# Optimization experiments

Measured on AMD Instinct MI355X. Metric: run time of the kernel, lower is better.

## Reference

```python
import jax, jax.numpy as jnp
import numpy as np
import math

D_MODEL = 2048
H = 16
Q_LORA = 1536
KV_LORA = 512
DN = 128   # qk_nope_head_dim
DR = 64    # qk_rope_head_dim
DV = 128   # v_head_dim
B, S = 2, 2048
EPS = 1e-5


def layernorm(x, g, b):
    mu = jnp.mean(x, axis=-1, keepdims=True)
    var = jnp.mean(jnp.square(x - mu), axis=-1, keepdims=True)
    return (x - mu) * jax.lax.rsqrt(var + EPS) * g + b


def rope_cos_sin(position_ids, dim):
    inv_freq = 1.0 / (10000.0 ** (jnp.arange(0, dim, 2, dtype=jnp.float32) / dim))
    ang = position_ids.astype(jnp.float32)[:, None] * inv_freq[None, :]  # [S, dim/2]
    return jnp.cos(ang), jnp.sin(ang)


def apply_rope(x, cos, sin):
    # x: [..., S, ..., dim]; cos/sin broadcastable [..., S, ..., dim/2]
    x1, x2 = jnp.split(x, 2, axis=-1)
    return jnp.concatenate([x1 * cos - x2 * sin, x1 * sin + x2 * cos], axis=-1)


def setup_inputs() -> dict:
    key = jax.random.key(0)
    ks = jax.random.split(key, 8)
    sc = 0.02
    return {
        "hidden_states": jax.random.normal(ks[0], (B, S, D_MODEL), jnp.float32),
        "w_qa": jax.random.normal(ks[1], (Q_LORA, D_MODEL), jnp.float32) * sc,
        "ln_qa_g": jnp.ones((Q_LORA,), jnp.float32),
        "ln_qa_b": jnp.zeros((Q_LORA,), jnp.float32),
        "w_qb": jax.random.normal(ks[2], (H * DN, Q_LORA), jnp.float32) * sc,
        "w_qrope": jax.random.normal(ks[3], (H * DR, Q_LORA), jnp.float32) * sc,
        "w_kva": jax.random.normal(ks[4], (KV_LORA + DR, D_MODEL), jnp.float32) * sc,
        "ln_kva_g": jnp.ones((KV_LORA,), jnp.float32),
        "ln_kva_b": jnp.zeros((KV_LORA,), jnp.float32),
        "w_kvb": jax.random.normal(ks[5], (H * (DN + DV), KV_LORA), jnp.float32) * sc,
        "w_o": jax.random.normal(ks[6], (D_MODEL, H * DV), jnp.float32) * sc,
        "position_ids": jnp.arange(S, dtype=jnp.int32),
    }


def reference(hidden_states, w_qa, ln_qa_g, ln_qa_b, w_qb, w_qrope,
              w_kva, ln_kva_g, ln_kva_b, w_kvb, w_o, position_ids):
    bsz, seq_len, _ = hidden_states.shape

    # --- Q path (low-rank) ---
    q_latent = layernorm(hidden_states @ w_qa.T, ln_qa_g, ln_qa_b)        # [B,S,Q_LORA]
    q_nope = (q_latent @ w_qb.T).reshape(bsz, seq_len, H, DN)             # [B,S,H,DN]
    q_rope = (q_latent @ w_qrope.T).reshape(bsz, seq_len, H, DR)          # [B,S,H,DR]

    # --- absorb k up-projection into q ---
    k_up = w_kvb[: H * DN].reshape(H, DN, KV_LORA)
    v_up = w_kvb[H * DN:].reshape(H, DV, KV_LORA)
    q_abs = jnp.einsum('bshd,hdr->bshr', q_nope, k_up)                    # [B,S,H,R]

    # --- KV latent path ---
    kv_mixed = hidden_states @ w_kva.T                                    # [B,S,R+DR]
    kv_latent = layernorm(kv_mixed[..., :KV_LORA], ln_kva_g, ln_kva_b)    # [B,S,R]
    k_rope = kv_mixed[..., KV_LORA:]                                      # [B,S,DR]

    # --- RoPE ---
    cos, sin = rope_cos_sin(position_ids, DR)                             # [S,DR/2]
    q_rope = apply_rope(q_rope, cos[None, :, None, :], sin[None, :, None, :])
    k_rope = apply_rope(k_rope, cos[None, :, :], sin[None, :, :])

    # --- attention over latent channel (keys shared across heads) ---
    q_full = jnp.concatenate([q_abs, q_rope], axis=-1)                    # [B,S,H,R+DR]
    k_full = jnp.concatenate([kv_latent, k_rope], axis=-1)                # [B,S,R+DR]
    scale = 1.0 / math.sqrt(DN + DR)
    scores = jnp.einsum('bqhc,bkc->bhqk', q_full, k_full) * scale
    probs = jax.nn.softmax(scores, axis=-1)
    attn = jnp.einsum('bhqk,bkr->bhqr', probs, kv_latent)                 # [B,H,S,R]

    # --- absorbed v up-projection + output ---
    attn_v = jnp.einsum('bhqr,hvr->bqhv', attn, v_up)                     # [B,S,H,DV]
    attn_v = attn_v.reshape(bsz, seq_len, H * DV)
    return attn_v @ w_o.T                                                 # [B,S,D_MODEL]
```

## Files before the change

kernel.cpp:

```cpp
#include <hip/hip_runtime.h>
#include <math.h>

#define D_MODEL 2048
#define NH 16
#define Q_LORA 1536
#define KV_LORA 512
#define DN 128
#define DR 64
#define DV 128
#define BB 2
#define SS 2048
#define NROWS (BB*SS)
#define LN_EPS 1e-5f

typedef __attribute__((ext_vector_type(8))) short short8;
typedef __attribute__((ext_vector_type(4))) float f32x4;

__device__ __forceinline__ ushort f2bf(float f) {
    unsigned int u = __float_as_uint(f);
    u = u + 0x7fffu + ((u >> 16) & 1u);
    return (ushort)(u >> 16);
}

__device__ __forceinline__ float fexp2(float x) {
#if __has_builtin(__builtin_amdgcn_exp2f)
    return __builtin_amdgcn_exp2f(x);
#else
    return exp2f(x);
#endif
}

__device__ __forceinline__ void cv4(const float* __restrict__ s,
                                    ushort* __restrict__ d, long i) {
    float4 v = ((const float4*)s)[i];
    ushort4 o;
    o.x = f2bf(v.x); o.y = f2bf(v.y); o.z = f2bf(v.z); o.w = f2bf(v.w);
    ((ushort4*)d)[i] = o;
}

__global__ __launch_bounds__(256)
void cvt_all(const float* __restrict__ hs,     const float* __restrict__ w_qa,
             const float* __restrict__ w_qb,   const float* __restrict__ w_qrope,
             const float* __restrict__ w_kvb,  const float* __restrict__ w_kva,
             ushort* __restrict__ hs_bf,       ushort* __restrict__ w_qa_bf,
             ushort* __restrict__ w_qb_bf,     ushort* __restrict__ w_qrope_bf,
             ushort* __restrict__ w_kvb_bf,    ushort* __restrict__ w_kva_bf,
             const int* __restrict__ pos,      float2* __restrict__ tab)
{
    long i = (long)blockIdx.x * 256 + threadIdx.x;
    if (i < 2097152) { cv4(hs, hs_bf, i); return; }
    i -= 2097152;
    if (i < 786432) { cv4(w_qa, w_qa_bf, i); return; }
    i -= 786432;
    if (i < 786432) { cv4(w_qb, w_qb_bf, i); return; }
    i -= 786432;
    if (i < 393216) { cv4(w_qrope, w_qrope_bf, i); return; }
    i -= 393216;
    if (i < 524288) { cv4(w_kvb, w_kvb_bf, i); return; }
    i -= 524288;
    if (i < 327680) {
        long e = i * 4;
        int row = (int)(e >> 11), col = (int)(e & 2047);
        ushort4 o;
        if (row < 576) {
            float4 v = *(const float4*)(w_kva + (long)row * 2048 + col);
            o.x = f2bf(v.x); o.y = f2bf(v.y); o.z = f2bf(v.z); o.w = f2bf(v.w);
        } else { o.x = 0; o.y = 0; o.z = 0; o.w = 0; }
        *(ushort4*)(w_kva_bf + (long)row * 2048 + col) = o;
        return;
    }
    i -= 327680;
    if (i >= 65536) return;
    int idx = (int)i;
    int fi = idx & 31;
    int s = idx >> 5;
    double ang = (double)pos[s] * exp(-(double)fi * 0.28782313662425572);
    float2 cs;
    cs.x = (float)cos(ang);
    cs.y = (float)sin(ang);
    tab[idx] = cs;
}

#define GLL16(g, l) \
    __builtin_amdgcn_global_load_lds((const __attribute__((address_space(1))) void*)(g), \
                                     (__attribute__((address_space(3))) void*)(l), 16, 0, 0)

__device__ __forceinline__ void gemm_core(const ushort* __restrict__ A,
    const ushort* __restrict__ Bp, ushort* As, ushort* Bs,
    int K, int lda, int ldb, int m0, int n0, int tid, f32x4 acc[4][4])
{
    int l = tid & 63, w = tid >> 6;
    int l15 = l & 15, quad = l >> 4;
    int wm = (w >> 1) * 64, wn = (w & 1) * 64;
    int ob = tid * 16;
    int row = ob >> 6, colb = ob & 63;
    const char* ga0 = (const char*)(A  + (long)(m0 + row) * lda)      + colb;
    const char* ga1 = (const char*)(A  + (long)(m0 + row + 64) * lda) + colb;
    const char* gb0 = (const char*)(Bp + (long)(n0 + row) * ldb)      + colb;
    const char* gb1 = (const char*)(Bp + (long)(n0 + row + 64) * ldb) + colb;
    ushort* la0 = As + tid * 8;
    ushort* la1 = As + 2048 + tid * 8;
    ushort* lb0 = Bs + tid * 8;
    ushort* lb1 = Bs + 2048 + tid * 8;

    for (int k0 = 0; k0 < K; k0 += 32) {
        GLL16(ga0, la0); GLL16(ga1, la1);
        GLL16(gb0, lb0); GLL16(gb1, lb1);
        ga0 += 64; ga1 += 64; gb0 += 64; gb1 += 64;
        __syncthreads();
        short8 af[4], bf[4];
        #pragma unroll
        for (int i = 0; i < 4; ++i)
            af[i] = *(const short8*)(As + (wm + i * 16 + l15) * 32 + quad * 8);
        #pragma unroll
        for (int j = 0; j < 4; ++j)
            bf[j] = *(const short8*)(Bs + (wn + j * 16 + l15) * 32 + quad * 8);
        #pragma unroll
        for (int i = 0; i < 4; ++i)
            #pragma unroll
            for (int j = 0; j < 4; ++j)
                acc[i][j] = __builtin_amdgcn_mfma_f32_16x16x32_bf16(
                    af[i], bf[j], acc[i][j], 0, 0, 0);
        __syncthreads();
    }
}

__global__ __launch_bounds__(256)
void gemm_f32out(const ushort* __restrict__ A, const ushort* __restrict__ B,
                 float* __restrict__ C, int K, int lda, int ldb, int ldc)
{
    __shared__ __align__(16) ushort As[128 * 32];
    __shared__ __align__(16) ushort Bs[128 * 32];
    int tid = threadIdx.x;
    int m0 = blockIdx.y * 128, n0 = blockIdx.x * 128;
    f32x4 acc[4][4] = {};
    gemm_core(A, B, As, Bs, K, lda, ldb, m0, n0, tid, acc);
    int l = tid & 63, w = tid >> 6;
    int l15 = l & 15, quad = l >> 4;
    int wm = (w >> 1) * 64, wn = (w & 1) * 64;
    #pragma unroll
    for (int i = 0; i < 4; ++i)
        #pragma unroll
        for (int j = 0; j < 4; ++j)
            #pragma unroll
            for (int r = 0; r < 4; ++r) {
                long gm = m0 + wm + i * 16 + quad * 4 + r;
                long gn = n0 + wn + j * 16 + l15;
                C[gm * ldc + gn] = acc[i][j][r];
            }
}

__global__ __launch_bounds__(256)
void gemm_dual(const ushort* __restrict__ A, const ushort* __restrict__ Bqa,
               const ushort* __restrict__ Bkva, float* __restrict__ Cq,
               float* __restrict__ Ckv)
{
    __shared__ __align__(16) ushort As[128 * 32];
    __shared__ __align__(16) ushort Bs[128 * 32];
    int tid = threadIdx.x;
    int bx = blockIdx.x;
    int m0 = blockIdx.y * 128;
    const ushort* Bp; float* C; int ldc, n0;
    if (bx < 12) { n0 = bx * 128;        Bp = Bqa  + (long)n0 * 2048; C = Cq;  ldc = 1536; }
    else         { n0 = (bx - 12) * 128; Bp = Bkva + (long)n0 * 2048; C = Ckv; ldc = 640; }
    f32x4 acc[4][4] = {};
    gemm_core(A, Bp, As, Bs, D_MODEL, D_MODEL, D_MODEL, m0, 0, tid, acc);
    int l = tid & 63, w = tid >> 6;
    int l15 = l & 15, quad = l >> 4;
    int wm = (w >> 1) * 64, wn = (w & 1) * 64;
    #pragma unroll
    for (int i = 0; i < 4; ++i)
        #pragma unroll
        for (int j = 0; j < 4; ++j)
            #pragma unroll
            for (int r = 0; r < 4; ++r) {
                long gm = m0 + wm + i * 16 + quad * 4 + r;
                long gn = n0 + wn + j * 16 + l15;
                C[gm * ldc + gn] = acc[i][j][r];
            }
}

__global__ __launch_bounds__(256)
void gemm_qkv(const ushort* __restrict__ Aq, const ushort* __restrict__ Bqb,
              const ushort* __restrict__ Bqr, ushort* __restrict__ qfull,
              const float2* __restrict__ tab,
              const ushort* __restrict__ Akv, const ushort* __restrict__ Bkvb,
              ushort* __restrict__ kfull, ushort* __restrict__ vt)
{
    __shared__ __align__(16) ushort As[128 * 32];
    __shared__ __align__(16) ushort Bs[128 * 32];
    int tid = threadIdx.x;
    int bx = blockIdx.x;
    int m0 = blockIdx.y * 128;
    int l = tid & 63, w = tid >> 6;
    int l15 = l & 15, quad = l >> 4;
    int wm = (w >> 1) * 64, wn = (w & 1) * 64;
    f32x4 acc[4][4] = {};

    if (bx < 24) {
        int n0 = bx * 128;
        const ushort* Bp = (n0 < 2048) ? Bqb + (long)n0 * Q_LORA
                                       : Bqr + (long)(n0 - 2048) * Q_LORA;
        gemm_core(Aq, Bp, As, Bs, Q_LORA, Q_LORA, Q_LORA, m0, 0, tid, acc);
        if (n0 < 2048) {
            int head = n0 >> 7;
            #pragma unroll
            for (int i = 0; i < 4; ++i)
                #pragma unroll
                for (int j = 0; j < 4; ++j)
                    #pragma unroll
                    for (int r = 0; r < 4; ++r) {
                        long gm = m0 + wm + i * 16 + quad * 4 + r;
                        int c = wn + j * 16 + l15;
                        qfull[(gm * NH + head) * 192 + c] = f2bf(acc[i][j][r]);
                    }
        } else {
            int nb = n0 - 2048;
            int head = (nb + wn) >> 6;
            #pragma unroll
            for (int i = 0; i < 4; ++i)
                #pragma unroll
                for (int j = 0; j < 2; ++j)
                    #pragma unroll
                    for (int r = 0; r < 4; ++r) {
                        long gm = m0 + wm + i * 16 + quad * 4 + r;
                        int ir = j * 16 + l15;
                        int s = (int)(gm & (SS - 1));
                        float2 cs = tab[s * 32 + ir];
                        float x1 = acc[i][j][r], x2 = acc[i][j + 2][r];
                        ushort* op = qfull + (gm * NH + head) * 192 + 128;
                        op[ir]      = f2bf(x1 * cs.x - x2 * cs.y);
                        op[ir + 32] = f2bf(x1 * cs.y + x2 * cs.x);
                    }
        }
    } else {
        int n0 = (bx - 24) * 128;
        const ushort* Bp = Bkvb + (long)n0 * KV_LORA;
        gemm_core(Akv, Bp, As, Bs, KV_LORA, KV_LORA, KV_LORA, m0, 0, tid, acc);
        if (n0 < 2048) {
            int head = n0 >> 7;
            #pragma unroll
            for (int i = 0; i < 4; ++i)
                #pragma unroll
                for (int j = 0; j < 4; ++j)
                    #pragma unroll
                    for (int r = 0; r < 4; ++r) {
                        long gm = m0 + wm + i * 16 + quad * 4 + r;
                        int c = wn + j * 16 + l15;
                        kfull[(gm * NH + head) * 192 + c] = f2bf(acc[i][j][r]);
                    }
        } else {
            int head = (n0 >> 7) - 16;
            #pragma unroll
            for (int i = 0; i < 4; ++i)
                #pragma unroll
                for (int j = 0; j < 4; ++j) {
                    long gm0 = m0 + wm + i * 16 + quad * 4;
                    int c = wn + j * 16 + l15;
                    ushort4 p;
                    p.x = f2bf(acc[i][j][0]); p.y = f2bf(acc[i][j][1]);
                    p.z = f2bf(acc[i][j][2]); p.w = f2bf(acc[i][j][3]);
                    *(ushort4*)(vt + (long)head * 128 * 4096 + (long)c * 4096 + gm0) = p;
                }
        }
    }
}

__global__ __launch_bounds__(256)
void ln_rope(const float* __restrict__ qlf, ushort* __restrict__ qlbf,
             const float* __restrict__ gqa, const float* __restrict__ bqa,
             const float* __restrict__ kvm, ushort* __restrict__ kvbf,
             const float* __restrict__ gkv, const float* __restrict__ bkv,
             ushort* __restrict__ kfull, const float2* __restrict__ tab,
             const float* __restrict__ w_o, ushort* __restrict__ w_o_bf)
{
    __shared__ float sred[4], ssred[4];
    int bid = blockIdx.x, tid = threadIdx.x;
    if (bid < 2 * NROWS) {
        const float* x; ushort* y; const float* g; const float* b; int n;
        if (bid < NROWS) {
            x = qlf + (long)bid * Q_LORA; y = qlbf + (long)bid * Q_LORA;
            g = gqa; b = bqa; n = Q_LORA;
        } else {
            int r = bid - NROWS;
            x = kvm + (long)r * 640; y = kvbf + (long)r * KV_LORA;
            g = gkv; b = bkv; n = KV_LORA;
        }
        float s = 0.f, ss = 0.f;
        for (int i = tid; i < n; i += 256) { float v = x[i]; s += v; ss += v * v; }
        #pragma unroll
        for (int off = 32; off > 0; off >>= 1) {
            s  += __shfl_xor(s, off);
            ss += __shfl_xor(ss, off);
        }
        int wid = tid >> 6, lane = tid & 63;
        if (lane == 0) { sred[wid] = s; ssred[wid] = ss; }
        __syncthreads();
        s  = sred[0] + sred[1] + sred[2] + sred[3];
        ss = ssred[0] + ssred[1] + ssred[2] + ssred[3];
        float mu  = s / n;
        float var = ss / n - mu * mu;
        float r = 1.0f / sqrtf(var + LN_EPS);
        for (int i = tid; i < n; i += 256)
            y[i] = f2bf((x[i] - mu) * r * g[i] + b[i]);
        return;
    }
    if (bid < 2 * NROWS + 512) {
        long idx = (long)(bid - 2 * NROWS) * 256 + tid;
        if (idx >= (long)NROWS * 32) return;
        int i = (int)(idx & 31);
        long rowi = idx >> 5;
        int s = (int)(rowi & (SS - 1));
        float2 cs = tab[s * 32 + i];
        float c = cs.x, sn = cs.y;
        const float* p = kvm + rowi * 640 + 512;
        float x1 = p[i], x2 = p[i + 32];
        ushort v1 = f2bf(x1 * c - x2 * sn);
        ushort v2 = f2bf(x1 * sn + x2 * c);
        ushort* o = kfull + rowi * NH * 192 + 128;
        #pragma unroll
        for (int h = 0; h < NH; ++h) {
            o[h * 192 + i]      = v1;
            o[h * 192 + i + 32] = v2;
        }
        return;
    }
    long i = (long)(bid - (2 * NROWS + 512)) * 256 + tid;
    if (i < 1048576) cv4(w_o, w_o_bf, i);
}

#define C2LOG 0.10412700456539414f
#define THR2  11.541560327111707f

__global__ __launch_bounds__(512, 4)
void flash_mfma(const ushort* __restrict__ qf, const ushort* __restrict__ kf,
                const ushort* __restrict__ vt, ushort* __restrict__ attnv)
{
    __shared__ __align__(16) ushort Ks[64 * 192];
    __shared__ __align__(16) ushort Vs[144 * 64];
    __shared__ __align__(16) ushort Ps[128 * 72];
    int tid = threadIdx.x;
    int w = tid >> 6, l = tid & 63, l15 = l & 15, quad = l >> 4;
    int bh = blockIdx.x;
    int b = bh >> 4, h = bh & 15;
    int q0 = blockIdx.y * 128;

    {
        int e = 8192 + tid * 2;
        ushort2 iv;
        iv.x = (e     < 8256) ? (ushort)0x3F80 : (ushort)0;
        iv.y = (e + 1 < 8256) ? (ushort)0x3F80 : (ushort)0;
        *(ushort2*)&Vs[e] = iv;
    }

    const ushort* qp = qf + ((long)(b * SS + q0 + 16 * w + l15) * NH + h) * 192 + quad * 8;
    short8 aq[6];
    #pragma unroll
    for (int kk = 0; kk < 6; ++kk) aq[kk] = *(const short8*)(qp + kk * 32);

    f32x4 o[8] = {};
    f32x4 osum = {};
    float mrow = -INFINITY;

    const ushort* kbase = kf + ((long)(b * SS) * NH + h) * 192;
    const ushort* vbase = vt + (long)h * 128 * 4096 + (long)b * SS;

    int r0k = tid >> 3, subk = tid & 7;
    int v0  = tid >> 2, subv = tid & 3;
    const ushort* kgp = kbase + (long)r0k * (NH * 192);
    const ushort* vgp = vbase + (long)v0 * 4096;

    short8 pk[3], pv[2];
    #pragma unroll
    for (int it = 0; it < 3; ++it)
        pk[it] = *(const short8*)(kgp + (subk + 8 * it) * 8);
    #pragma unroll
    for (int it = 0; it < 2; ++it)
        pv[it] = *(const short8*)(vgp + (subv + 4 * it) * 8);

    int ksw = r0k & 7, vsw = v0 & 7;

    for (int k0 = 0; k0 < SS; k0 += 64) {
        __syncthreads();
        #pragma unroll
        for (int it = 0; it < 3; ++it)
            *(short8*)&Ks[r0k * 192 + ((subk + 8 * it) ^ ksw) * 8] = pk[it];
        #pragma unroll
        for (int it = 0; it < 2; ++it)
            *(short8*)&Vs[v0 * 64 + ((subv + 4 * it) ^ vsw) * 8] = pv[it];
        __syncthreads();
        if (k0 + 64 < SS) {
            const ushort* kg = kgp + (long)(k0 + 64) * (NH * 192);
            const ushort* vg = vgp + (k0 + 64);
            #pragma unroll
            for (int it = 0; it < 3; ++it)
                pk[it] = *(const short8*)(kg + (subk + 8 * it) * 8);
            #pragma unroll
            for (int it = 0; it < 2; ++it)
                pv[it] = *(const short8*)(vg + (subv + 4 * it) * 8);
        }

        f32x4 sc[4] = {};
        __builtin_amdgcn_s_setprio(1);
        #pragma unroll
        for (int kk = 0; kk < 6; ++kk) {
            #pragma unroll
            for (int j = 0; j < 4; ++j) {
                int krow = j * 16 + l15;
                short8 kfr = *(const short8*)&Ks[krow * 192 + (((kk * 4 + quad) ^ (krow & 7))) * 8];
                sc[j] = __builtin_amdgcn_mfma_f32_16x16x32_bf16(kfr, aq[kk], sc[j], 0, 0, 0);
            }
        }
        __builtin_amdgcn_s_setprio(0);

        float rmax = fmaxf(
            fmaxf(fmaxf(fmaxf(sc[0][0], sc[0][1]), fmaxf(sc[0][2], sc[0][3])),
                  fmaxf(fmaxf(sc[1][0], sc[1][1]), fmaxf(sc[1][2], sc[1][3]))),
            fmaxf(fmaxf(fmaxf(sc[2][0], sc[2][1]), fmaxf(sc[2][2], sc[2][3])),
                  fmaxf(fmaxf(sc[3][0], sc[3][1]), fmaxf(sc[3][2], sc[3][3]))));
        rmax = fmaxf(rmax, __shfl_xor(rmax, 16));
        rmax = fmaxf(rmax, __shfl_xor(rmax, 32));
        float pmax = rmax * C2LOG;

        if (__any(pmax > mrow + THR2)) {
            float mnew = fmaxf(mrow, pmax);
            float alpha = fexp2(mrow - mnew);
            mrow = mnew;
            float a0 = __shfl(alpha, quad * 4 + 0);
            float a1 = __shfl(alpha, quad * 4 + 1);
            float a2 = __shfl(alpha, quad * 4 + 2);
            float a3 = __shfl(alpha, quad * 4 + 3);
            #pragma unroll
            for (int v8 = 0; v8 < 8; ++v8) {
                o[v8][0] *= a0; o[v8][1] *= a1;
                o[v8][2] *= a2; o[v8][3] *= a3;
            }
            osum[0] *= a0; osum[1] *= a1; osum[2] *= a2; osum[3] *= a3;
        }

        int prow = (16 * w + l15) * 72 + quad * 4;
        #pragma unroll
        for (int j = 0; j < 4; ++j) {
            float p0 = fexp2(fmaf(sc[j][0], C2LOG, -mrow));
            float p1 = fexp2(fmaf(sc[j][1], C2LOG, -mrow));
            float p2 = fexp2(fmaf(sc[j][2], C2LOG, -mrow));
            float p3 = fexp2(fmaf(sc[j][3], C2LOG, -mrow));
            uint2 pu;
            pu.x = (uint)f2bf(p0) | ((uint)f2bf(p1) << 16);
            pu.y = (uint)f2bf(p2) | ((uint)f2bf(p3) << 16);
            *(uint2*)&Ps[prow + j * 16] = pu;
        }

        __builtin_amdgcn_s_setprio(1);
        #pragma unroll
        for (int ks = 0; ks < 2; ++ks) {
            short8 pa = *(const short8*)&Ps[(16 * w + l15) * 72 + ks * 32 + quad * 8];
            #pragma unroll
            for (int v8 = 0; v8 < 8; ++v8) {
                int vrow = v8 * 16 + l15;
                short8 bv = *(const short8*)&Vs[vrow * 64 + (((ks * 4 + quad) ^ (vrow & 7))) * 8];
                o[v8] = __builtin_amdgcn_mfma_f32_16x16x32_bf16(pa, bv, o[v8], 0, 0, 0);
            }
            {
                int vrow = 128 + l15;
                short8 bv = *(const short8*)&Vs[vrow * 64 + (((ks * 4 + quad) ^ (vrow & 7))) * 8];
                osum = __builtin_amdgcn_mfma_f32_16x16x32_bf16(pa, bv, osum, 0, 0, 0);
            }
        }
        __builtin_amdgcn_s_setprio(0);
    }

    #pragma unroll
    for (int r = 0; r < 4; ++r) {
        float lsum = __shfl(osum[r], l & 48);
        float inv = 1.0f / lsum;
        long rowi = (long)(b * SS) + q0 + 16 * w + quad * 4 + r;
        ushort* op = attnv + (rowi * NH + h) * 128;
        #pragma unroll
        for (int v8 = 0; v8 < 8; ++v8)
            op[v8 * 16 + l15] = f2bf(o[v8][r] * inv);
    }
}


extern "C" void kernel_launch(void* const* d_in, const int* in_sizes, int n_in,
                              void* d_out, int out_size, void* d_ws, size_t ws_size,
                              hipStream_t stream) {
    const float* hs       = (const float*)d_in[0];
    const float* w_qa     = (const float*)d_in[1];
    const float* ln_qa_g  = (const float*)d_in[2];
    const float* ln_qa_b  = (const float*)d_in[3];
    const float* w_qb     = (const float*)d_in[4];
    const float* w_qrope  = (const float*)d_in[5];
    const float* w_kva    = (const float*)d_in[6];
    const float* ln_kva_g = (const float*)d_in[7];
    const float* ln_kva_b = (const float*)d_in[8];
    const float* w_kvb    = (const float*)d_in[9];
    const float* w_o      = (const float*)d_in[10];
    const int*   pos      = (const int*)d_in[11];
    float* out = (float*)d_out;

    char* W = (char*)d_ws;
    ushort* hs_bf     = (ushort*)(W + 0);
    ushort* w_o_bf    = (ushort*)(W + 0);
    ushort* w_qa_bf   = (ushort*)(W + 16777216);
    ushort* w_qb_bf   = (ushort*)(W + 23068672);
    ushort* w_qrope_bf= (ushort*)(W + 29360128);
    ushort* w_kva_bf  = (ushort*)(W + 32505856);
    ushort* w_kvb_bf  = (ushort*)(W + 35127296);
    float*  q_lat_f   = (float*)(W + 39321600);
    ushort* q_lat_bf  = (ushort*)(W + 64487424);
    float*  kv_mix    = (float*)(W + 77070336);
    ushort* kv_lat_bf = (ushort*)(W + 87556096);
    ushort* q_full    = (ushort*)(W + 91750400);
    ushort* k_full    = (ushort*)(W + 116916224);
    ushort* v_exp_t   = (ushort*)(W + 142082048);
    ushort* attnv_bf  = (ushort*)(W + 158859264);
    float2* rope_tab  = (float2*)(W + 158859264);

    dim3 blk(256);

    cvt_all<<<dim3(19456), blk, 0, stream>>>(
        hs, w_qa, w_qb, w_qrope, w_kvb, w_kva,
        hs_bf, w_qa_bf, w_qb_bf, w_qrope_bf, w_kvb_bf, w_kva_bf,
        pos, rope_tab);
    gemm_dual<<<dim3(17, 32), blk, 0, stream>>>(
        hs_bf, w_qa_bf, w_kva_bf, q_lat_f, kv_mix);
    ln_rope<<<dim3(12800), blk, 0, stream>>>(
        q_lat_f, q_lat_bf, ln_qa_g, ln_qa_b,
        kv_mix, kv_lat_bf, ln_kva_g, ln_kva_b,
        k_full, rope_tab, w_o, w_o_bf);
    gemm_qkv<<<dim3(56, 32), blk, 0, stream>>>(
        q_lat_bf, w_qb_bf, w_qrope_bf, q_full, rope_tab,
        kv_lat_bf, w_kvb_bf, k_full, v_exp_t);
    flash_mfma<<<dim3(BB * NH, SS / 128), dim3(512), 0, stream>>>(
        q_full, k_full, v_exp_t, attnv_bf);
    gemm_f32out<<<dim3(16, 32), blk, 0, stream>>>(
        attnv_bf, w_o_bf, out, NH * DV, NH * DV, NH * DV, D_MODEL);
}
```

Before: 503.7 us.

## Double GEMM K-step with swizzled LDS tiles; compute softmax row sums with shuffles

The shared GEMM core now loads 64-wide K slices per iteration, with an XOR swizzle on the LDS column groups. This halves the number of barrier pairs per K and is meant to cut LDS bank conflicts on fragment reads. In exchange, LDS per block doubles, which may reduce occupancy. The flash kernel drops the extra ones-row MFMA used to accumulate softmax denominators and sums probabilities in registers with cross-lane shuffles. This removes MFMA work and LDS reads but adds VALU and shuffle work, and the sum is taken on fp32 probabilities rather than bf16-rounded ones.

```diff
diff --git a/kernel.cpp b/kernel.cpp
--- a/kernel.cpp
+++ b/kernel.cpp
@@ -92,35 +92,51 @@
     int l = tid & 63, w = tid >> 6;
     int l15 = l & 15, quad = l >> 4;
     int wm = (w >> 1) * 64, wn = (w & 1) * 64;
-    int ob = tid * 16;
-    int row = ob >> 6, colb = ob & 63;
-    const char* ga0 = (const char*)(A  + (long)(m0 + row) * lda)      + colb;
-    const char* ga1 = (const char*)(A  + (long)(m0 + row + 64) * lda) + colb;
-    const char* gb0 = (const char*)(Bp + (long)(n0 + row) * ldb)      + colb;
-    const char* gb1 = (const char*)(Bp + (long)(n0 + row + 64) * ldb) + colb;
+    int row = tid >> 3;
+    int cg  = ((tid & 7) ^ (row & 7)) * 8;
+    const char* ga0 = (const char*)(A  + (long)(m0 + row) * lda + cg);
+    const char* ga1 = (const char*)(A  + (long)(m0 + row + 32) * lda + cg);
+    const char* ga2 = (const char*)(A  + (long)(m0 + row + 64) * lda + cg);
+    const char* ga3 = (const char*)(A  + (long)(m0 + row + 96) * lda + cg);
+    const char* gb0 = (const char*)(Bp + (long)(n0 + row) * ldb + cg);
+    const char* gb1 = (const char*)(Bp + (long)(n0 + row + 32) * ldb + cg);
+    const char* gb2 = (const char*)(Bp + (long)(n0 + row + 64) * ldb + cg);
+    const char* gb3 = (const char*)(Bp + (long)(n0 + row + 96) * ldb + cg);
     ushort* la0 = As + tid * 8;
     ushort* la1 = As + 2048 + tid * 8;
+    ushort* la2 = As + 4096 + tid * 8;
+    ushort* la3 = As + 6144 + tid * 8;
     ushort* lb0 = Bs + tid * 8;
     ushort* lb1 = Bs + 2048 + tid * 8;
-
-    for (int k0 = 0; k0 < K; k0 += 32) {
-        GLL16(ga0, la0); GLL16(ga1, la1);
-        GLL16(gb0, lb0); GLL16(gb1, lb1);
-        ga0 += 64; ga1 += 64; gb0 += 64; gb1 += 64;
+    ushort* lb2 = Bs + 4096 + tid * 8;
+    ushort* lb3 = Bs + 6144 + tid * 8;
+
+    for (int k0 = 0; k0 < K; k0 += 64) {
+        GLL16(ga0, la0); GLL16(ga1, la1); GLL16(ga2, la2); GLL16(ga3, la3);
+        GLL16(gb0, lb0); GLL16(gb1, lb1); GLL16(gb2, lb2); GLL16(gb3, lb3);
+        ga0 += 128; ga1 += 128; ga2 += 128; ga3 += 128;
+        gb0 += 128; gb1 += 128; gb2 += 128; gb3 += 128;
         __syncthreads();
-        short8 af[4], bf[4];
-        #pragma unroll
-        for (int i = 0; i < 4; ++i)
-            af[i] = *(const short8*)(As + (wm + i * 16 + l15) * 32 + quad * 8);
-        #pragma unroll
-        for (int j = 0; j < 4; ++j)
-            bf[j] = *(const short8*)(Bs + (wn + j * 16 + l15) * 32 + quad * 8);
-        #pragma unroll
-        for (int i = 0; i < 4; ++i)
-            #pragma unroll
-            for (int j = 0; j < 4; ++j)
-                acc[i][j] = __builtin_amdgcn_mfma_f32_16x16x32_bf16(
-                    af[i], bf[j], acc[i][j], 0, 0, 0);
+        #pragma unroll
+        for (int half = 0; half < 2; ++half) {
+            short8 af[4], bf[4];
+            #pragma unroll
+            for (int i = 0; i < 4; ++i) {
+                int r = wm + i * 16 + l15;
+                af[i] = *(const short8*)(As + r * 64 + ((half * 4 + quad) ^ (l15 & 7)) * 8);
+            }
+            #pragma unroll
+            for (int j = 0; j < 4; ++j) {
+                int r = wn + j * 16 + l15;
+                bf[j] = *(const short8*)(Bs + r * 64 + ((half * 4 + quad) ^ (l15 & 7)) * 8);
+            }
+            #pragma unroll
+            for (int i = 0; i < 4; ++i)
+                #pragma unroll
+                for (int j = 0; j < 4; ++j)
+                    acc[i][j] = __builtin_amdgcn_mfma_f32_16x16x32_bf16(
+                        af[i], bf[j], acc[i][j], 0, 0, 0);
+        }
         __syncthreads();
     }
 }
@@ -129,8 +145,8 @@
 void gemm_f32out(const ushort* __restrict__ A, const ushort* __restrict__ B,
                  float* __restrict__ C, int K, int lda, int ldb, int ldc)
 {
-    __shared__ __align__(16) ushort As[128 * 32];
-    __shared__ __align__(16) ushort Bs[128 * 32];
+    __shared__ __align__(16) ushort As[128 * 64];
+    __shared__ __align__(16) ushort Bs[128 * 64];
     int tid = threadIdx.x;
     int m0 = blockIdx.y * 128, n0 = blockIdx.x * 128;
     f32x4 acc[4][4] = {};
@@ -155,8 +171,8 @@
                const ushort* __restrict__ Bkva, float* __restrict__ Cq,
                float* __restrict__ Ckv)
 {
-    __shared__ __align__(16) ushort As[128 * 32];
-    __shared__ __align__(16) ushort Bs[128 * 32];
+    __shared__ __align__(16) ushort As[128 * 64];
+    __shared__ __align__(16) ushort Bs[128 * 64];
     int tid = threadIdx.x;
     int bx = blockIdx.x;
     int m0 = blockIdx.y * 128;
@@ -187,8 +203,8 @@
               const ushort* __restrict__ Akv, const ushort* __restrict__ Bkvb,
               ushort* __restrict__ kfull, ushort* __restrict__ vt)
 {
-    __shared__ __align__(16) ushort As[128 * 32];
-    __shared__ __align__(16) ushort Bs[128 * 32];
+    __shared__ __align__(16) ushort As[128 * 64];
+    __shared__ __align__(16) ushort Bs[128 * 64];
     int tid = threadIdx.x;
     int bx = blockIdx.x;
     int m0 = blockIdx.y * 128;
@@ -337,7 +353,7 @@
                 const ushort* __restrict__ vt, ushort* __restrict__ attnv)
 {
     __shared__ __align__(16) ushort Ks[64 * 192];
-    __shared__ __align__(16) ushort Vs[144 * 64];
+    __shared__ __align__(16) ushort Vs[128 * 64];
     __shared__ __align__(16) ushort Ps[128 * 72];
     int tid = threadIdx.x;
     int w = tid >> 6, l = tid & 63, l15 = l & 15, quad = l >> 4;
@@ -345,21 +361,13 @@
     int b = bh >> 4, h = bh & 15;
     int q0 = blockIdx.y * 128;
 
-    {
-        int e = 8192 + tid * 2;
-        ushort2 iv;
-        iv.x = (e     < 8256) ? (ushort)0x3F80 : (ushort)0;
-        iv.y = (e + 1 < 8256) ? (ushort)0x3F80 : (ushort)0;
-        *(ushort2*)&Vs[e] = iv;
-    }
-
     const ushort* qp = qf + ((long)(b * SS + q0 + 16 * w + l15) * NH + h) * 192 + quad * 8;
     short8 aq[6];
     #pragma unroll
     for (int kk = 0; kk < 6; ++kk) aq[kk] = *(const short8*)(qp + kk * 32);
 
     f32x4 o[8] = {};
-    f32x4 osum = {};
+    float lsum = 0.f;
     float mrow = -INFINITY;
 
     const ushort* kbase = kf + ((long)(b * SS) * NH + h) * 192;
@@ -426,6 +434,7 @@
             float mnew = fmaxf(mrow, pmax);
             float alpha = fexp2(mrow - mnew);
             mrow = mnew;
+            lsum *= alpha;
             float a0 = __shfl(alpha, quad * 4 + 0);
             float a1 = __shfl(alpha, quad * 4 + 1);
             float a2 = __shfl(alpha, quad * 4 + 2);
@@ -435,9 +444,9 @@
                 o[v8][0] *= a0; o[v8][1] *= a1;
                 o[v8][2] *= a2; o[v8][3] *= a3;
             }
-            osum[0] *= a0; osum[1] *= a1; osum[2] *= a2; osum[3] *= a3;
-        }
-
+        }
+
+        float tsum = 0.f;
         int prow = (16 * w + l15) * 72 + quad * 4;
         #pragma unroll
         for (int j = 0; j < 4; ++j) {
@@ -445,11 +454,15 @@
             float p1 = fexp2(fmaf(sc[j][1], C2LOG, -mrow));
             float p2 = fexp2(fmaf(sc[j][2], C2LOG, -mrow));
             float p3 = fexp2(fmaf(sc[j][3], C2LOG, -mrow));
+            tsum += (p0 + p1) + (p2 + p3);
             uint2 pu;
             pu.x = (uint)f2bf(p0) | ((uint)f2bf(p1) << 16);
             pu.y = (uint)f2bf(p2) | ((uint)f2bf(p3) << 16);
             *(uint2*)&Ps[prow + j * 16] = pu;
         }
+        tsum += __shfl_xor(tsum, 16);
+        tsum += __shfl_xor(tsum, 32);
+        lsum += tsum;
 
         __builtin_amdgcn_s_setprio(1);
         #pragma unroll
@@ -461,19 +474,14 @@
                 short8 bv = *(const short8*)&Vs[vrow * 64 + (((ks * 4 + quad) ^ (vrow & 7))) * 8];
                 o[v8] = __builtin_amdgcn_mfma_f32_16x16x32_bf16(pa, bv, o[v8], 0, 0, 0);
             }
-            {
-                int vrow = 128 + l15;
-                short8 bv = *(const short8*)&Vs[vrow * 64 + (((ks * 4 + quad) ^ (vrow & 7))) * 8];
-                osum = __builtin_amdgcn_mfma_f32_16x16x32_bf16(pa, bv, osum, 0, 0, 0);
-            }
         }
         __builtin_amdgcn_s_setprio(0);
     }
 
     #pragma unroll
     for (int r = 0; r < 4; ++r) {
-        float lsum = __shfl(osum[r], l & 48);
-        float inv = 1.0f / lsum;
+        float Lq = __shfl(lsum, quad * 4 + r);
+        float inv = 1.0f / Lq;
         long rowi = (long)(b * SS) + q0 + 16 * w + quad * 4 + r;
         ushort* op = attnv + (rowi * NH + h) * 128;
         #pragma unroll
```

After: 483.3 us. 1.04x faster.
